# Kernel optimization log

Measured on AMD Instinct MI355X. Metric: run time of the kernel, lower is better.

The kernel has to match this reference:

```python
import jax, jax.numpy as jnp
import numpy as np

S, N, DIN, DH, C, K, E = 12, 50000, 64, 128, 2, 3, 600000
HID = (DH + C) // 2  # 65
LN_EPS = 1e-5


def setup_inputs() -> dict:
    key = jax.random.key(0)
    ks = jax.random.split(key, 16)
    sc = 0.05
    inp = {
        'H': jax.random.normal(ks[0], (S, N, DIN), dtype=jnp.float32),
        'edge_index': jax.random.randint(ks[1], (2, E), 0, N, dtype=jnp.int64),
        # stacked gate params, gate order: 0=i, 1=f, 2=c(cell), 3=o
        'Wx': jax.random.normal(ks[2], (4, K, DIN, DH), dtype=jnp.float32) * sc,
        'bx': jnp.zeros((4, DH), dtype=jnp.float32),
        'Wh': jax.random.normal(ks[3], (4, K, DH, DH), dtype=jnp.float32) * sc,
        'bh': jnp.zeros((4, DH), dtype=jnp.float32),
        'b_gate': jnp.zeros((4, DH), dtype=jnp.float32),
        'wc': jax.random.normal(ks[4], (3, DH), dtype=jnp.float32) * sc,  # peephole: i, f, o
        'ln_gamma': jnp.ones((DH,), dtype=jnp.float32),
        'ln_beta': jnp.zeros((DH,), dtype=jnp.float32),
        'W1': jax.random.normal(ks[5], (DH, HID), dtype=jnp.float32) * sc,
        'b1': jnp.zeros((HID,), dtype=jnp.float32),
        'W2': jax.random.normal(ks[6], (HID, C), dtype=jnp.float32) * sc,
        'b2': jnp.zeros((C,), dtype=jnp.float32),
    }
    return inp


def _cheb_norm(edge_index):
    # sym-normalized, lambda_max=2 => scaled Laplacian Lhat = -D^-1/2 A D^-1/2 (zero diagonal)
    src, dst = edge_index[0], edge_index[1]
    ones = jnp.ones((src.shape[0],), dtype=jnp.float32)
    deg = jax.ops.segment_sum(ones, src, num_segments=N)
    dinv = jnp.where(deg > 0, jax.lax.rsqrt(jnp.maximum(deg, 1.0)), 0.0)
    norm = -dinv[src] * dinv[dst]
    return src, dst, norm


def _cheb_conv(x, W, b, src, dst, norm):
    # x: [N, Din]; W: [K, Din, Dout]. T0=x, T1=Lhat x, Tk=2 Lhat T_{k-1} - T_{k-2}
    Tx0 = x
    out = Tx0 @ W[0]
    if K > 1:
        Tx1 = jax.ops.segment_sum(norm[:, None] * Tx0[src], dst, num_segments=N)
        out = out + Tx1 @ W[1]
        for k in range(2, K):
            Tx2 = 2.0 * jax.ops.segment_sum(norm[:, None] * Tx1[src], dst, num_segments=N) - Tx0
            out = out + Tx2 @ W[k]
            Tx0, Tx1 = Tx1, Tx2
    return out + b


def _decoder(H, edge_index, Wx, bx, Wh, bh, b_gate, wc, ln_gamma, ln_beta, W1, b1, W2, b2):
    src, dst, norm = _cheb_norm(edge_index)

    def step(carry, x_t):
        h, c = carry
        gx = lambda g: _cheb_conv(x_t, Wx[g], bx[g], src, dst, norm)
        gh = lambda g: _cheb_conv(h, Wh[g], bh[g], src, dst, norm)
        i = jax.nn.sigmoid(gx(0) + gh(0) + wc[0] * c + b_gate[0])
        f = jax.nn.sigmoid(gx(1) + gh(1) + wc[1] * c + b_gate[1])
        t = jnp.tanh(gx(2) + gh(2) + b_gate[2])
        c = f * c + i * t
        o = jax.nn.sigmoid(gx(3) + gh(3) + wc[2] * c + b_gate[3])
        h = o * jnp.tanh(c)
        return (h, c), h

    h0 = jnp.zeros((N, DH), dtype=H.dtype)
    (_, _), X = jax.lax.scan(step, (h0, h0), H)  # X: [S, N, DH]

    X = jnp.tanh(X)
    # LayerNorm over conv_dim (last axis here)
    mu = jnp.mean(X, axis=-1, keepdims=True)
    var = jnp.mean(jnp.square(X - mu), axis=-1, keepdims=True)
    X = (X - mu) * jax.lax.rsqrt(var + LN_EPS) * ln_gamma + ln_beta
    # dropout in eval mode: identity
    X = jax.nn.relu(X @ W1 + b1) @ W2 + b2  # [S, N, C]
    X = jax.nn.sigmoid(X)
    return jnp.transpose(X, (1, 2, 0))  # [N, C, S]


def reference(H, edge_index, Wx, bx, Wh, bh, b_gate, wc, ln_gamma, ln_beta, W1, b1, W2, b2):
    return _decoder(H, edge_index, Wx, bx, Wh, bh, b_gate, wc, ln_gamma, ln_beta, W1, b1, W2, b2)
```

## Files before the change

kernel.cpp:

```cpp
#include <hip/hip_runtime.h>
#include <cstdint>
#include <cstddef>

#define S_DIM 12
#define N_NODE 50000
#define N_PAD 50048
#define N_P2 50176
#define D_IN 64
#define D_H 128
#define N_E 600000
#define K_TOT 576
#define N_COL 512
#define HID_P 80
#define N_HID 65
#define AXC 192

typedef short bf16x8 __attribute__((ext_vector_type(8)));
typedef float f32x4 __attribute__((ext_vector_type(4)));

__device__ __forceinline__ float bf2f(unsigned short u){
  union { unsigned int i; float f; } v; v.i = ((unsigned int)u) << 16; return v.f;
}
__device__ __forceinline__ unsigned short f2bf(float f){
  union { float f; unsigned int i; } v; v.f = f;
  unsigned int x = v.i;
  return (unsigned short)((x + 0x7fffu + ((x >> 16) & 1u)) >> 16);
}
__device__ __forceinline__ float sigf(float x){ return 1.f/(1.f + __expf(-x)); }
__device__ __forceinline__ float ftanh(float x){
  x = fminf(fmaxf(x, -12.f), 12.f);
  float e = __expf(2.f*x);
  return (e - 1.f)/(e + 1.f);
}

__device__ __forceinline__ void gload16(const void* g, void* lds){
  __builtin_amdgcn_global_load_lds((const __attribute__((address_space(1))) unsigned int*)g,
                                   (__attribute__((address_space(3))) unsigned int*)lds, 16, 0, 0);
}

__device__ __forceinline__ void acc12(float* a, uint2 p0, uint2 p1, uint2 p2, float w){
  unsigned int u[6] = {p0.x, p0.y, p1.x, p1.y, p2.x, p2.y};
#pragma unroll
  for (int i=0;i<6;++i){
    a[2*i]   += w * bf2f((unsigned short)(u[i] & 0xffffu));
    a[2*i+1] += w * bf2f((unsigned short)(u[i] >> 16));
  }
}
__device__ __forceinline__ void acc8(float* a, uint4 h, float w){
  unsigned int u[4] = {h.x, h.y, h.z, h.w};
#pragma unroll
  for (int i=0;i<4;++i){
    a[2*i]   += w * bf2f((unsigned short)(u[i] & 0xffffu));
    a[2*i+1] += w * bf2f((unsigned short)(u[i] >> 16));
  }
}

__global__ void k_prep(const float* __restrict__ Wx, const float* __restrict__ Wh,
                       const float* __restrict__ bx, const float* __restrict__ bh,
                       const float* __restrict__ bg, const float* __restrict__ W1,
                       const float* __restrict__ b1, const float* __restrict__ W2,
                       unsigned short* __restrict__ Bct, float* __restrict__ btot,
                       unsigned short* __restrict__ W1t, float* __restrict__ b1p,
                       float* __restrict__ W2p)
{
  int idx = blockIdx.x*256 + threadIdx.x;
  if (idx < N_COL*K_TOT){
    int cc = idx / K_TOT, k = idx - cc*K_TOT;
    int g = (cc>>4)&3, d = (cc&15) + ((cc>>6)<<4);
    float v;
    if (k < 384){
      int kt = k >> 7, j = k & 127;
      const float* Wg = Wh + (size_t)g*3*128*128;
      if (kt == 0)      v = Wg[(size_t)j*128 + d] - Wg[(size_t)(256+j)*128 + d];
      else if (kt == 1) v = Wg[(size_t)(128+j)*128 + d];
      else              v = 2.f*Wg[(size_t)(256+j)*128 + d];
    } else {
      int kk = k - 384; int kt = kk >> 6, j = kk & 63;
      const float* Wg = Wx + (size_t)g*3*64*128;
      if (kt == 0)      v = Wg[(size_t)j*128 + d] - Wg[(size_t)(128+j)*128 + d];
      else if (kt == 1) v = Wg[(size_t)(64+j)*128 + d];
      else              v = 2.f*Wg[(size_t)(128+j)*128 + d];
    }
    Bct[(size_t)cc*K_TOT + k] = f2bf(v);
  }
  if (idx < N_COL) btot[idx] = bx[idx] + bh[idx] + bg[idx];
  if (idx < HID_P*D_H){ int c = idx >> 7, k = idx & 127;
    W1t[idx] = (c < N_HID) ? f2bf(W1[k*N_HID + c]) : (unsigned short)0; }
  if (idx < HID_P) b1p[idx] = (idx < N_HID) ? b1[idx] : 0.f;
  if (idx < HID_P*2){ int c = idx >> 1, j = idx & 1; W2p[idx] = (c < N_HID) ? W2[c*2 + j] : 0.f; }
}

__global__ void k_xprep(const float* __restrict__ H, unsigned short* __restrict__ Xtr,
                        unsigned short* __restrict__ Axt){
  int idx = blockIdx.x*256 + threadIdx.x;
  if (idx >= N_PAD*64) return;
  int n = idx >> 6, d = idx & 63;
  union { unsigned short u[12]; uint2 q[3]; } pk;
  if (n < N_NODE){
#pragma unroll
    for (int t=0;t<12;++t) pk.u[t] = f2bf(H[((size_t)t*N_NODE + n)*64 + d]);
  } else {
#pragma unroll
    for (int t=0;t<12;++t) pk.u[t] = 0;
  }
  uint2* xp = (uint2*)(Xtr + (size_t)idx*12);
  xp[0]=pk.q[0]; xp[1]=pk.q[1]; xp[2]=pk.q[2];
#pragma unroll
  for (int t=0;t<12;++t) Axt[((size_t)t*N_PAD + n)*AXC + d] = pk.u[t];
  if (n >= N_NODE){
#pragma unroll
    for (int t=0;t<12;++t){
      Axt[((size_t)t*N_PAD + n)*AXC + 64 + d]  = 0;
      Axt[((size_t)t*N_PAD + n)*AXC + 128 + d] = 0;
    }
  }
}

__global__ void k_deg(const int* __restrict__ ei, int* __restrict__ dsrc, int* __restrict__ ddst){
  int e = blockIdx.x*256 + threadIdx.x;
  if (e < N_E){
    atomicAdd(&dsrc[ei[e]], 1);
    atomicAdd(&ddst[ei[N_E + e]], 1);
  }
}
__global__ void k_dinv(const int* __restrict__ dsrc, float* __restrict__ dinv){
  int n = blockIdx.x*256 + threadIdx.x;
  if (n < N_P2) dinv[n] = (dsrc[n] > 0) ? rsqrtf((float)dsrc[n]) : 0.f;
}
__global__ void k_scan1(const int* __restrict__ in, int* __restrict__ outp, int* __restrict__ part){
  __shared__ int sm[256];
  int tid = threadIdx.x;
  int i = blockIdx.x*256 + tid;
  int v = in[i];
  int x = v;
  sm[tid] = x; __syncthreads();
  for (int off=1; off<256; off<<=1){
    int y = (tid >= off) ? sm[tid-off] : 0;
    __syncthreads();
    x += y; sm[tid] = x; __syncthreads();
  }
  outp[i] = x - v;
  if (tid == 255) part[blockIdx.x] = x;
}
__global__ void k_scan2(int* __restrict__ part, int nblk){
  __shared__ int sm[256];
  int tid = threadIdx.x;
  int v = (tid < nblk) ? part[tid] : 0;
  int x = v; sm[tid] = x; __syncthreads();
  for (int off=1; off<256; off<<=1){
    int y = (tid >= off) ? sm[tid-off] : 0;
    __syncthreads();
    x += y; sm[tid] = x; __syncthreads();
  }
  if (tid < nblk) part[tid] = x - v;
}
__global__ void k_scan3(const int* __restrict__ outp, const int* __restrict__ part, int* __restrict__ offs){
  int i = blockIdx.x*256 + threadIdx.x;
  offs[i] = outp[i] + part[blockIdx.x];
}
__global__ void k_csr(const int* __restrict__ ei, const float* __restrict__ dinv,
                      const int* __restrict__ offs, int* __restrict__ cursor,
                      int2* __restrict__ cedge){
  int e = blockIdx.x*256 + threadIdx.x;
  if (e < N_E){
    int s = ei[e], d = ei[N_E + e];
    int pos = atomicAdd(&cursor[d], 1);
    float w = -dinv[s]*dinv[d];
    cedge[offs[d] + pos] = make_int2(s, __float_as_int(w));
  }
}

__global__ void k_xspmm1(const unsigned short* __restrict__ Xtr, unsigned short* __restrict__ Axt,
                         unsigned short* __restrict__ U1tr,
                         const int* __restrict__ offs, const int2* __restrict__ cedge){
  int n = blockIdx.x*4 + (threadIdx.x >> 6);
  int l = threadIdx.x & 63;
  if (n >= N_NODE) return;
  int beg = offs[n], end = offs[n+1];
  float a[12];
#pragma unroll
  for (int t=0;t<12;++t) a[t] = 0.f;
  for (int q = beg; q < end; q += 3){
    int2 e0 = cedge[q];
    int2 e1 = (q+1 < end) ? cedge[q+1] : make_int2(0,0);
    int2 e2 = (q+2 < end) ? cedge[q+2] : make_int2(0,0);
    const uint2* r0 = (const uint2*)(Xtr + ((size_t)e0.x*64 + l)*12);
    const uint2* r1 = (const uint2*)(Xtr + ((size_t)e1.x*64 + l)*12);
    const uint2* r2 = (const uint2*)(Xtr + ((size_t)e2.x*64 + l)*12);
    uint2 p00=r0[0], p01=r0[1], p02=r0[2];
    uint2 p10=r1[0], p11=r1[1], p12=r1[2];
    uint2 p20=r2[0], p21=r2[1], p22=r2[2];
    acc12(a, p00, p01, p02, __int_as_float(e0.y));
    acc12(a, p10, p11, p12, __int_as_float(e1.y));
    acc12(a, p20, p21, p22, __int_as_float(e2.y));
  }
  union { unsigned short u[12]; uint2 qq[3]; } pk;
#pragma unroll
  for (int t=0;t<12;++t){
    unsigned short b = f2bf(a[t]);
    pk.u[t] = b;
    Axt[((size_t)t*N_PAD + n)*AXC + 64 + l] = b;
  }
  uint2* op = (uint2*)(U1tr + ((size_t)n*64 + l)*12);
  op[0]=pk.qq[0]; op[1]=pk.qq[1]; op[2]=pk.qq[2];
}
__global__ void k_xspmm2(const unsigned short* __restrict__ U1tr, unsigned short* __restrict__ Axt,
                         const int* __restrict__ offs, const int2* __restrict__ cedge){
  int n = blockIdx.x*4 + (threadIdx.x >> 6);
  int l = threadIdx.x & 63;
  if (n >= N_NODE) return;
  int beg = offs[n], end = offs[n+1];
  float a[12];
#pragma unroll
  for (int t=0;t<12;++t) a[t] = 0.f;
  for (int q = beg; q < end; q += 3){
    int2 e0 = cedge[q];
    int2 e1 = (q+1 < end) ? cedge[q+1] : make_int2(0,0);
    int2 e2 = (q+2 < end) ? cedge[q+2] : make_int2(0,0);
    const uint2* r0 = (const uint2*)(U1tr + ((size_t)e0.x*64 + l)*12);
    const uint2* r1 = (const uint2*)(U1tr + ((size_t)e1.x*64 + l)*12);
    const uint2* r2 = (const uint2*)(U1tr + ((size_t)e2.x*64 + l)*12);
    uint2 p00=r0[0], p01=r0[1], p02=r0[2];
    uint2 p10=r1[0], p11=r1[1], p12=r1[2];
    uint2 p20=r2[0], p21=r2[1], p22=r2[2];
    acc12(a, p00, p01, p02, __int_as_float(e0.y));
    acc12(a, p10, p11, p12, __int_as_float(e1.y));
    acc12(a, p20, p21, p22, __int_as_float(e2.y));
  }
#pragma unroll
  for (int t=0;t<12;++t)
    Axt[((size_t)t*N_PAD + n)*AXC + 128 + l] = f2bf(a[t]);
}

__global__ void k_spmm1(const unsigned short* __restrict__ Hc, unsigned short* __restrict__ U,
                        const int* __restrict__ offs, const int2* __restrict__ cedge){
  int n = blockIdx.x*4 + (threadIdx.x >> 6);
  int l = threadIdx.x & 63;
  if (n >= N_NODE) return;
  int sub = l >> 4, fl = l & 15;
  int beg = offs[n], end = offs[n+1];
  float a[8];
#pragma unroll
  for (int j=0;j<8;++j) a[j] = 0.f;
  for (int q = beg; q < end; q += 8){
    int i0 = q + sub, i1 = q + 4 + sub;
    int2 e0 = (i0 < end) ? cedge[i0] : make_int2(0,0);
    int2 e1 = (i1 < end) ? cedge[i1] : make_int2(0,0);
    uint4 h0 = *(const uint4*)(Hc + (size_t)e0.x*128 + fl*8);
    uint4 h1 = *(const uint4*)(Hc + (size_t)e1.x*128 + fl*8);
    acc8(a, h0, __int_as_float(e0.y));
    acc8(a, h1, __int_as_float(e1.y));
  }
#pragma unroll
  for (int j=0;j<8;++j){
    a[j] += __shfl_xor(a[j], 16);
    a[j] += __shfl_xor(a[j], 32);
  }
  if (sub == 0){
    unsigned short o[8];
#pragma unroll
    for (int j=0;j<8;++j) o[j] = f2bf(a[j]);
    *(uint4*)(U + (size_t)n*256 + fl*8) = *(const uint4*)o;
  }
}
__global__ void k_spmm2(unsigned short* __restrict__ U,
                        const int* __restrict__ offs, const int2* __restrict__ cedge){
  int n = blockIdx.x*4 + (threadIdx.x >> 6);
  int l = threadIdx.x & 63;
  if (n >= N_NODE) return;
  int sub = l >> 4, fl = l & 15;
  int beg = offs[n], end = offs[n+1];
  float a[8];
#pragma unroll
  for (int j=0;j<8;++j) a[j] = 0.f;
  for (int q = beg; q < end; q += 8){
    int i0 = q + sub, i1 = q + 4 + sub;
    int2 e0 = (i0 < end) ? cedge[i0] : make_int2(0,0);
    int2 e1 = (i1 < end) ? cedge[i1] : make_int2(0,0);
    uint4 h0 = *(const uint4*)(U + (size_t)e0.x*256 + fl*8);
    uint4 h1 = *(const uint4*)(U + (size_t)e1.x*256 + fl*8);
    acc8(a, h0, __int_as_float(e0.y));
    acc8(a, h1, __int_as_float(e1.y));
  }
#pragma unroll
  for (int j=0;j<8;++j){
    a[j] += __shfl_xor(a[j], 16);
    a[j] += __shfl_xor(a[j], 32);
  }
  if (sub == 0){
    unsigned short o[8];
#pragma unroll
    for (int j=0;j<8;++j) o[j] = f2bf(a[j]);
    *(uint4*)(U + (size_t)n*256 + 128 + fl*8) = *(const uint4*)o;
  }
}

__global__ __launch_bounds__(256,2) void k_gemm(
    const unsigned short* __restrict__ Hc, const unsigned short* __restrict__ U,
    const unsigned short* __restrict__ Axt,
    const unsigned short* __restrict__ Bct, const float* __restrict__ btot,
    const float* __restrict__ wc, float* __restrict__ c, unsigned short* __restrict__ Hn)
{
  __shared__ __align__(16) unsigned short As[128*64];
  __shared__ __align__(16) unsigned short Bs[128*64];
  int tid = threadIdx.x;
  int w = tid >> 6, l = tid & 63;
  const int NWG = 1564, q8 = NWG >> 3, r8 = NWG & 7;
  int L = blockIdx.y*4 + blockIdx.x;
  int xcd = L & 7, li = L >> 3;
  int W = (xcd < r8 ? xcd*(q8+1) : r8*(q8+1) + (xcd-r8)*q8) + li;
  int bx = W & 3, by = W >> 2;
  int n0 = bx * 128;
  int m0 = by * 128;
  const f32x4 vzero = {0.f,0.f,0.f,0.f};
  f32x4 acc[4][4];
#pragma unroll
  for (int i=0;i<4;++i)
#pragma unroll
    for (int j=0;j<4;++j) acc[i][j] = vzero;
  int wr = w >> 1, wn = w & 1;
  for (int it=0; it<9; ++it){
    const unsigned short* Ab; int astr, acol;
    if (it < 2)      { Ab = Hc;  astr = 128; acol = it*64; }
    else if (it < 6) { Ab = U;   astr = 256; acol = (it-2)*64; }
    else             { Ab = Axt; astr = AXC; acol = (it-6)*64; }
    if (it) __syncthreads();
#pragma unroll
    for (int i=0;i<4;++i){
      int rr = w*32 + i*8;
      int row = rr + (l>>3);
      gload16(Ab  + (size_t)(m0+row)*astr + acol + (l&7)*8, (void*)(As + rr*64));
      gload16(Bct + (size_t)(n0+row)*K_TOT + it*64 + (l&7)*8, (void*)(Bs + rr*64));
    }
    __syncthreads();
#pragma unroll
    for (int kk=0; kk<2; ++kk){
      bf16x8 af[4], bfv[4];
#pragma unroll
      for (int i=0;i<4;++i) af[i]  = *(const bf16x8*)(As + (wr*64 + i*16 + (l&15))*64 + kk*32 + (l>>4)*8);
#pragma unroll
      for (int j=0;j<4;++j) bfv[j] = *(const bf16x8*)(Bs + (wn*64 + j*16 + (l&15))*64 + kk*32 + (l>>4)*8);
#pragma unroll
      for (int i=0;i<4;++i)
#pragma unroll
        for (int j=0;j<4;++j)
          acc[i][j] = __builtin_amdgcn_mfma_f32_16x16x32_bf16(af[i], bfv[j], acc[i][j], 0,0,0);
    }
  }
  int dd = (((bx<<1) + wn) << 4) | (l & 15);
  float b_i = btot[dd], b_f = btot[128+dd], b_t = btot[256+dd], b_o = btot[384+dd];
  float wci = wc[dd], wcf = wc[128+dd], wco = wc[256+dd];
#pragma unroll
  for (int i=0;i<4;++i){
    int row0 = m0 + wr*64 + i*16 + (l>>4)*4;
#pragma unroll
    for (int r=0;r<4;++r){
      int row = row0 + r;
      float co = c[(size_t)row*128 + dd];
      float gi = sigf(acc[i][0][r] + b_i + wci*co);
      float gf = sigf(acc[i][1][r] + b_f + wcf*co);
      float tt = ftanh(acc[i][2][r] + b_t);
      float cn = gf*co + gi*tt;
      float go = sigf(acc[i][3][r] + b_o + wco*cn);
      float h = go * ftanh(cn);
      c[(size_t)row*128 + dd] = cn;
      Hn[(size_t)row*128 + dd] = f2bf(h);
    }
  }
}

__global__ __launch_bounds__(256,2) void k_lnmlp(const unsigned short* __restrict__ Hn,
                        const unsigned short* __restrict__ W1t, const float* __restrict__ b1p,
                        const float* __restrict__ W2p, const float* __restrict__ b2,
                        const float* __restrict__ gam, const float* __restrict__ bet,
                        float* __restrict__ out, int t)
{
  __shared__ __align__(16) unsigned short xn[64*128];
  __shared__ __align__(16) unsigned short w1s[HID_P*128];
  __shared__ float w2s[HID_P*2];
  __shared__ float b1s[HID_P];
  __shared__ float b2s[2];
  int tid = threadIdx.x;
  for (int i = tid; i < HID_P*128/8; i += 256) ((int4*)w1s)[i] = ((const int4*)W1t)[i];
  if (tid < HID_P*2) w2s[tid] = W2p[tid];
  if (tid < HID_P)   b1s[tid] = b1p[tid];
  if (tid < 2)       b2s[tid] = b2[tid];
  int n0 = blockIdx.x*64;
  int row = tid >> 2, part = tid & 3;
  int n = n0 + row;
  float vals[32];
  float s = 0.f, ss = 0.f;
  if (n < N_NODE){
    const unsigned short* hp = Hn + (size_t)n*128 + part*32;
#pragma unroll
    for (int k=0;k<32;++k){
      float x = ftanh(bf2f(hp[k]));
      vals[k] = x; s += x; ss += x*x;
    }
  } else {
#pragma unroll
    for (int k=0;k<32;++k) vals[k] = 0.f;
  }
  s  += __shfl_xor(s,1);  s  += __shfl_xor(s,2);
  ss += __shfl_xor(ss,1); ss += __shfl_xor(ss,2);
  float mu = s * (1.f/128.f);
  float var = ss * (1.f/128.f) - mu*mu;
  float inv = rsqrtf(fmaxf(var, 0.f) + 1e-5f);
#pragma unroll
  for (int k=0;k<32;++k){
    int d = part*32 + k;
    xn[row*128 + d] = f2bf((vals[k]-mu)*inv*gam[d] + bet[d]);
  }
  __syncthreads();
  int w = tid >> 6, l = tid & 63;
  const f32x4 vzero = {0.f,0.f,0.f,0.f};
  f32x4 acc[5];
#pragma unroll
  for (int tj=0;tj<5;++tj) acc[tj] = vzero;
#pragma unroll
  for (int kk=0;kk<4;++kk){
    bf16x8 a = *(const bf16x8*)(xn + (w*16 + (l&15))*128 + kk*32 + (l>>4)*8);
#pragma unroll
    for (int tj=0;tj<5;++tj){
      bf16x8 b = *(const bf16x8*)(w1s + (tj*16 + (l&15))*128 + kk*32 + (l>>4)*8);
      acc[tj] = __builtin_amdgcn_mfma_f32_16x16x32_bf16(a, b, acc[tj], 0,0,0);
    }
  }
#pragma unroll
  for (int r=0;r<4;++r){
    int rn = n0 + w*16 + (l>>4)*4 + r;
    float p0 = 0.f, p1 = 0.f;
#pragma unroll
    for (int tj=0;tj<5;++tj){
      int col = tj*16 + (l&15);
      float hv = fmaxf(acc[tj][r] + b1s[col], 0.f);
      p0 += hv * w2s[col*2];
      p1 += hv * w2s[col*2+1];
    }
    p0 += __shfl_xor(p0,1); p0 += __shfl_xor(p0,2); p0 += __shfl_xor(p0,4); p0 += __shfl_xor(p0,8);
    p1 += __shfl_xor(p1,1); p1 += __shfl_xor(p1,2); p1 += __shfl_xor(p1,4); p1 += __shfl_xor(p1,8);
    if ((l & 15) == 0 && rn < N_NODE){
      float* op = out + (size_t)rn*24 + t;
      op[0]  = sigf(p0 + b2s[0]);
      op[12] = sigf(p1 + b2s[1]);
    }
  }
}

extern "C" void kernel_launch(void* const* d_in, const int* in_sizes, int n_in,
                              void* d_out, int out_size, void* d_ws, size_t ws_size,
                              hipStream_t stream)
{
  const float* H   = (const float*)d_in[0];
  const int*   ei  = (const int*)d_in[1];
  const float* Wx  = (const float*)d_in[2];
  const float* bx  = (const float*)d_in[3];
  const float* Wh  = (const float*)d_in[4];
  const float* bh  = (const float*)d_in[5];
  const float* bg  = (const float*)d_in[6];
  const float* wc  = (const float*)d_in[7];
  const float* gam = (const float*)d_in[8];
  const float* bet = (const float*)d_in[9];
  const float* W1  = (const float*)d_in[10];
  const float* b1  = (const float*)d_in[11];
  const float* W2  = (const float*)d_in[12];
  const float* b2  = (const float*)d_in[13];
  float* out = (float*)d_out;
  (void)in_sizes; (void)n_in; (void)out_size; (void)ws_size;

  char* p = (char*)d_ws;
  auto alloc = [&](size_t bytes)->char*{ char* r = p; p += (bytes + 255) & ~(size_t)255; return r; };
  char* zbase = p;
  float*          c_st  = (float*)alloc((size_t)N_PAD*128*4);
  unsigned short* Hbuf0 = (unsigned short*)alloc((size_t)N_PAD*128*2);
  int* dsrc   = (int*)alloc((size_t)N_P2*4);
  int* ddst   = (int*)alloc((size_t)N_P2*4);
  int* cursor = (int*)alloc((size_t)N_P2*4);
  size_t zbytes = (size_t)(p - zbase);
  unsigned short* Hbuf1 = (unsigned short*)alloc((size_t)N_PAD*128*2);
  unsigned short* Ubuf  = (unsigned short*)alloc((size_t)N_PAD*256*2);
  unsigned short* Xtr   = (unsigned short*)alloc((size_t)N_PAD*64*12*2);
  unsigned short* U1tr  = (unsigned short*)alloc((size_t)N_PAD*64*12*2);
  unsigned short* Axt   = (unsigned short*)alloc((size_t)S_DIM*N_PAD*AXC*2);
  unsigned short* Bct   = (unsigned short*)alloc((size_t)N_COL*K_TOT*2);
  float*          btot  = (float*)alloc(N_COL*4);
  unsigned short* W1t   = (unsigned short*)alloc(HID_P*128*2);
  float*          b1p   = (float*)alloc(HID_P*4);
  float*          W2p   = (float*)alloc(HID_P*2*4);
  float*          dinv  = (float*)alloc((size_t)N_P2*4);
  int*            offs  = (int*)alloc((size_t)(N_P2+256)*4);
  int*            outp  = (int*)alloc((size_t)N_P2*4);
  int*            partb = (int*)alloc(256*4);
  int2*           cedge = (int2*)alloc((size_t)N_E*8);

  hipMemsetAsync(zbase, 0, zbytes, stream);
  k_prep<<<(N_COL*K_TOT + 255)/256, 256, 0, stream>>>(Wx, Wh, bx, bh, bg, W1, b1, W2,
                                                      Bct, btot, W1t, b1p, W2p);
  k_xprep<<<(N_PAD*64 + 255)/256, 256, 0, stream>>>(H, Xtr, Axt);
  k_deg<<<(N_E + 255)/256, 256, 0, stream>>>(ei, dsrc, ddst);
  k_dinv<<<N_P2/256, 256, 0, stream>>>(dsrc, dinv);
  k_scan1<<<N_P2/256, 256, 0, stream>>>(ddst, outp, partb);
  k_scan2<<<1, 256, 0, stream>>>(partb, N_P2/256);
  k_scan3<<<N_P2/256, 256, 0, stream>>>(outp, partb, offs);
  k_csr<<<(N_E + 255)/256, 256, 0, stream>>>(ei, dinv, offs, cursor, cedge);
  k_xspmm1<<<N_NODE/4, 256, 0, stream>>>(Xtr, Axt, U1tr, offs, cedge);
  k_xspmm2<<<N_NODE/4, 256, 0, stream>>>(U1tr, Axt, offs, cedge);

  for (int t = 0; t < S_DIM; ++t){
    unsigned short* Hc = (t & 1) ? Hbuf1 : Hbuf0;
    unsigned short* Hn = (t & 1) ? Hbuf0 : Hbuf1;
    k_spmm1<<<N_NODE/4, 256, 0, stream>>>(Hc, Ubuf, offs, cedge);
    k_spmm2<<<N_NODE/4, 256, 0, stream>>>(Ubuf, offs, cedge);
    k_gemm<<<dim3(4, N_PAD/128), 256, 0, stream>>>(Hc, Ubuf,
        Axt + (size_t)t*N_PAD*AXC, Bct, btot, wc, c_st, Hn);
    k_lnmlp<<<N_PAD/64, 256, 0, stream>>>(Hn, W1t, b1p, W2p, b2, gam, bet, out, t);
  }
}
```

Measured before the change: 1.973 ms.

## Unroll SpMM gathers, double-buffer GEMM LDS tiles, skip first-step hidden SpMM

The CSR gather loops in the four SpMM kernels now process twice as many edges per iteration, using clamped indices and zeroed weights in place of conditional loads, so more gathers are in flight. The GEMM gets double-buffered shared-memory tiles so the next K-slice loads while MFMAs run on the current one, with one barrier per iteration. At t=0 the hidden-state SpMMs are skipped because h0 is zero, and Ubuf is moved into the memset region so its zeros stand in for them. The trade-off is more registers and twice the LDS per block, which may lower occupancy under launch_bounds(256,2).

```diff
diff --git a/kernel.cpp b/kernel.cpp
--- a/kernel.cpp
+++ b/kernel.cpp
@@ -177,22 +177,41 @@
   int l = threadIdx.x & 63;
   if (n >= N_NODE) return;
   int beg = offs[n], end = offs[n+1];
+  int ce = end - 1;
   float a[12];
 #pragma unroll
   for (int t=0;t<12;++t) a[t] = 0.f;
-  for (int q = beg; q < end; q += 3){
-    int2 e0 = cedge[q];
-    int2 e1 = (q+1 < end) ? cedge[q+1] : make_int2(0,0);
-    int2 e2 = (q+2 < end) ? cedge[q+2] : make_int2(0,0);
+  for (int q = beg; q < end; q += 6){
+    int2 e0 = cedge[min(q,   ce)];
+    int2 e1 = cedge[min(q+1, ce)];
+    int2 e2 = cedge[min(q+2, ce)];
+    int2 e3 = cedge[min(q+3, ce)];
+    int2 e4 = cedge[min(q+4, ce)];
+    int2 e5 = cedge[min(q+5, ce)];
+    float w0 = __int_as_float(e0.y);
+    float w1 = (q+1 < end) ? __int_as_float(e1.y) : 0.f;
+    float w2 = (q+2 < end) ? __int_as_float(e2.y) : 0.f;
+    float w3 = (q+3 < end) ? __int_as_float(e3.y) : 0.f;
+    float w4 = (q+4 < end) ? __int_as_float(e4.y) : 0.f;
+    float w5 = (q+5 < end) ? __int_as_float(e5.y) : 0.f;
     const uint2* r0 = (const uint2*)(Xtr + ((size_t)e0.x*64 + l)*12);
     const uint2* r1 = (const uint2*)(Xtr + ((size_t)e1.x*64 + l)*12);
     const uint2* r2 = (const uint2*)(Xtr + ((size_t)e2.x*64 + l)*12);
+    const uint2* r3 = (const uint2*)(Xtr + ((size_t)e3.x*64 + l)*12);
+    const uint2* r4 = (const uint2*)(Xtr + ((size_t)e4.x*64 + l)*12);
+    const uint2* r5 = (const uint2*)(Xtr + ((size_t)e5.x*64 + l)*12);
     uint2 p00=r0[0], p01=r0[1], p02=r0[2];
     uint2 p10=r1[0], p11=r1[1], p12=r1[2];
     uint2 p20=r2[0], p21=r2[1], p22=r2[2];
-    acc12(a, p00, p01, p02, __int_as_float(e0.y));
-    acc12(a, p10, p11, p12, __int_as_float(e1.y));
-    acc12(a, p20, p21, p22, __int_as_float(e2.y));
+    uint2 p30=r3[0], p31=r3[1], p32=r3[2];
+    uint2 p40=r4[0], p41=r4[1], p42=r4[2];
+    uint2 p50=r5[0], p51=r5[1], p52=r5[2];
+    acc12(a, p00, p01, p02, w0);
+    acc12(a, p10, p11, p12, w1);
+    acc12(a, p20, p21, p22, w2);
+    acc12(a, p30, p31, p32, w3);
+    acc12(a, p40, p41, p42, w4);
+    acc12(a, p50, p51, p52, w5);
   }
   union { unsigned short u[12]; uint2 qq[3]; } pk;
 #pragma unroll
@@ -210,22 +229,41 @@
   int l = threadIdx.x & 63;
   if (n >= N_NODE) return;
   int beg = offs[n], end = offs[n+1];
+  int ce = end - 1;
   float a[12];
 #pragma unroll
   for (int t=0;t<12;++t) a[t] = 0.f;
-  for (int q = beg; q < end; q += 3){
-    int2 e0 = cedge[q];
-    int2 e1 = (q+1 < end) ? cedge[q+1] : make_int2(0,0);
-    int2 e2 = (q+2 < end) ? cedge[q+2] : make_int2(0,0);
+  for (int q = beg; q < end; q += 6){
+    int2 e0 = cedge[min(q,   ce)];
+    int2 e1 = cedge[min(q+1, ce)];
+    int2 e2 = cedge[min(q+2, ce)];
+    int2 e3 = cedge[min(q+3, ce)];
+    int2 e4 = cedge[min(q+4, ce)];
+    int2 e5 = cedge[min(q+5, ce)];
+    float w0 = __int_as_float(e0.y);
+    float w1 = (q+1 < end) ? __int_as_float(e1.y) : 0.f;
+    float w2 = (q+2 < end) ? __int_as_float(e2.y) : 0.f;
+    float w3 = (q+3 < end) ? __int_as_float(e3.y) : 0.f;
+    float w4 = (q+4 < end) ? __int_as_float(e4.y) : 0.f;
+    float w5 = (q+5 < end) ? __int_as_float(e5.y) : 0.f;
     const uint2* r0 = (const uint2*)(U1tr + ((size_t)e0.x*64 + l)*12);
     const uint2* r1 = (const uint2*)(U1tr + ((size_t)e1.x*64 + l)*12);
     const uint2* r2 = (const uint2*)(U1tr + ((size_t)e2.x*64 + l)*12);
+    const uint2* r3 = (const uint2*)(U1tr + ((size_t)e3.x*64 + l)*12);
+    const uint2* r4 = (const uint2*)(U1tr + ((size_t)e4.x*64 + l)*12);
+    const uint2* r5 = (const uint2*)(U1tr + ((size_t)e5.x*64 + l)*12);
     uint2 p00=r0[0], p01=r0[1], p02=r0[2];
     uint2 p10=r1[0], p11=r1[1], p12=r1[2];
     uint2 p20=r2[0], p21=r2[1], p22=r2[2];
-    acc12(a, p00, p01, p02, __int_as_float(e0.y));
-    acc12(a, p10, p11, p12, __int_as_float(e1.y));
-    acc12(a, p20, p21, p22, __int_as_float(e2.y));
+    uint2 p30=r3[0], p31=r3[1], p32=r3[2];
+    uint2 p40=r4[0], p41=r4[1], p42=r4[2];
+    uint2 p50=r5[0], p51=r5[1], p52=r5[2];
+    acc12(a, p00, p01, p02, w0);
+    acc12(a, p10, p11, p12, w1);
+    acc12(a, p20, p21, p22, w2);
+    acc12(a, p30, p31, p32, w3);
+    acc12(a, p40, p41, p42, w4);
+    acc12(a, p50, p51, p52, w5);
   }
 #pragma unroll
   for (int t=0;t<12;++t)
@@ -239,17 +277,28 @@
   if (n >= N_NODE) return;
   int sub = l >> 4, fl = l & 15;
   int beg = offs[n], end = offs[n+1];
+  int ce = end - 1;
   float a[8];
 #pragma unroll
   for (int j=0;j<8;++j) a[j] = 0.f;
-  for (int q = beg; q < end; q += 8){
-    int i0 = q + sub, i1 = q + 4 + sub;
-    int2 e0 = (i0 < end) ? cedge[i0] : make_int2(0,0);
-    int2 e1 = (i1 < end) ? cedge[i1] : make_int2(0,0);
+  for (int q = beg; q < end; q += 16){
+    int i0 = q + sub, i1 = q + 4 + sub, i2 = q + 8 + sub, i3 = q + 12 + sub;
+    int2 e0 = cedge[min(i0, ce)];
+    int2 e1 = cedge[min(i1, ce)];
+    int2 e2 = cedge[min(i2, ce)];
+    int2 e3 = cedge[min(i3, ce)];
+    float w0 = (i0 < end) ? __int_as_float(e0.y) : 0.f;
+    float w1 = (i1 < end) ? __int_as_float(e1.y) : 0.f;
+    float w2 = (i2 < end) ? __int_as_float(e2.y) : 0.f;
+    float w3 = (i3 < end) ? __int_as_float(e3.y) : 0.f;
     uint4 h0 = *(const uint4*)(Hc + (size_t)e0.x*128 + fl*8);
     uint4 h1 = *(const uint4*)(Hc + (size_t)e1.x*128 + fl*8);
-    acc8(a, h0, __int_as_float(e0.y));
-    acc8(a, h1, __int_as_float(e1.y));
+    uint4 h2 = *(const uint4*)(Hc + (size_t)e2.x*128 + fl*8);
+    uint4 h3 = *(const uint4*)(Hc + (size_t)e3.x*128 + fl*8);
+    acc8(a, h0, w0);
+    acc8(a, h1, w1);
+    acc8(a, h2, w2);
+    acc8(a, h3, w3);
   }
 #pragma unroll
   for (int j=0;j<8;++j){
@@ -270,17 +319,28 @@
   if (n >= N_NODE) return;
   int sub = l >> 4, fl = l & 15;
   int beg = offs[n], end = offs[n+1];
+  int ce = end - 1;
   float a[8];
 #pragma unroll
   for (int j=0;j<8;++j) a[j] = 0.f;
-  for (int q = beg; q < end; q += 8){
-    int i0 = q + sub, i1 = q + 4 + sub;
-    int2 e0 = (i0 < end) ? cedge[i0] : make_int2(0,0);
-    int2 e1 = (i1 < end) ? cedge[i1] : make_int2(0,0);
+  for (int q = beg; q < end; q += 16){
+    int i0 = q + sub, i1 = q + 4 + sub, i2 = q + 8 + sub, i3 = q + 12 + sub;
+    int2 e0 = cedge[min(i0, ce)];
+    int2 e1 = cedge[min(i1, ce)];
+    int2 e2 = cedge[min(i2, ce)];
+    int2 e3 = cedge[min(i3, ce)];
+    float w0 = (i0 < end) ? __int_as_float(e0.y) : 0.f;
+    float w1 = (i1 < end) ? __int_as_float(e1.y) : 0.f;
+    float w2 = (i2 < end) ? __int_as_float(e2.y) : 0.f;
+    float w3 = (i3 < end) ? __int_as_float(e3.y) : 0.f;
     uint4 h0 = *(const uint4*)(U + (size_t)e0.x*256 + fl*8);
     uint4 h1 = *(const uint4*)(U + (size_t)e1.x*256 + fl*8);
-    acc8(a, h0, __int_as_float(e0.y));
-    acc8(a, h1, __int_as_float(e1.y));
+    uint4 h2 = *(const uint4*)(U + (size_t)e2.x*256 + fl*8);
+    uint4 h3 = *(const uint4*)(U + (size_t)e3.x*256 + fl*8);
+    acc8(a, h0, w0);
+    acc8(a, h1, w1);
+    acc8(a, h2, w2);
+    acc8(a, h3, w3);
   }
 #pragma unroll
   for (int j=0;j<8;++j){
@@ -301,8 +361,8 @@
     const unsigned short* __restrict__ Bct, const float* __restrict__ btot,
     const float* __restrict__ wc, float* __restrict__ c, unsigned short* __restrict__ Hn)
 {
-  __shared__ __align__(16) unsigned short As[128*64];
-  __shared__ __align__(16) unsigned short Bs[128*64];
+  __shared__ __align__(16) unsigned short As[2][128*64];
+  __shared__ __align__(16) unsigned short Bs[2][128*64];
   int tid = threadIdx.x;
   int w = tid >> 6, l = tid & 63;
   const int NWG = 1564, q8 = NWG >> 3, r8 = NWG & 7;
@@ -319,33 +379,40 @@
 #pragma unroll
     for (int j=0;j<4;++j) acc[i][j] = vzero;
   int wr = w >> 1, wn = w & 1;
-  for (int it=0; it<9; ++it){
+
+  auto stage = [&](int buf, int it){
     const unsigned short* Ab; int astr, acol;
     if (it < 2)      { Ab = Hc;  astr = 128; acol = it*64; }
     else if (it < 6) { Ab = U;   astr = 256; acol = (it-2)*64; }
     else             { Ab = Axt; astr = AXC; acol = (it-6)*64; }
-    if (it) __syncthreads();
 #pragma unroll
     for (int i=0;i<4;++i){
       int rr = w*32 + i*8;
       int row = rr + (l>>3);
-      gload16(Ab  + (size_t)(m0+row)*astr + acol + (l&7)*8, (void*)(As + rr*64));
-      gload16(Bct + (size_t)(n0+row)*K_TOT + it*64 + (l&7)*8, (void*)(Bs + rr*64));
-    }
-    __syncthreads();
+      gload16(Ab  + (size_t)(m0+row)*astr + acol + (l&7)*8, (void*)(As[buf] + rr*64));
+      gload16(Bct + (size_t)(n0+row)*K_TOT + it*64 + (l&7)*8, (void*)(Bs[buf] + rr*64));
+    }
+  };
+
+  stage(0, 0);
+  __syncthreads();
+  for (int it=0; it<9; ++it){
+    int cur = it & 1;
+    if (it < 8) stage(cur^1, it+1);
 #pragma unroll
     for (int kk=0; kk<2; ++kk){
       bf16x8 af[4], bfv[4];
 #pragma unroll
-      for (int i=0;i<4;++i) af[i]  = *(const bf16x8*)(As + (wr*64 + i*16 + (l&15))*64 + kk*32 + (l>>4)*8);
-#pragma unroll
-      for (int j=0;j<4;++j) bfv[j] = *(const bf16x8*)(Bs + (wn*64 + j*16 + (l&15))*64 + kk*32 + (l>>4)*8);
+      for (int i=0;i<4;++i) af[i]  = *(const bf16x8*)(As[cur] + (wr*64 + i*16 + (l&15))*64 + kk*32 + (l>>4)*8);
+#pragma unroll
+      for (int j=0;j<4;++j) bfv[j] = *(const bf16x8*)(Bs[cur] + (wn*64 + j*16 + (l&15))*64 + kk*32 + (l>>4)*8);
 #pragma unroll
       for (int i=0;i<4;++i)
 #pragma unroll
         for (int j=0;j<4;++j)
           acc[i][j] = __builtin_amdgcn_mfma_f32_16x16x32_bf16(af[i], bfv[j], acc[i][j], 0,0,0);
     }
+    __syncthreads();
   }
   int dd = (((bx<<1) + wn) << 4) | (l & 15);
   float b_i = btot[dd], b_f = btot[128+dd], b_t = btot[256+dd], b_o = btot[384+dd];
@@ -473,12 +540,12 @@
   char* zbase = p;
   float*          c_st  = (float*)alloc((size_t)N_PAD*128*4);
   unsigned short* Hbuf0 = (unsigned short*)alloc((size_t)N_PAD*128*2);
+  unsigned short* Ubuf  = (unsigned short*)alloc((size_t)N_PAD*256*2);
   int* dsrc   = (int*)alloc((size_t)N_P2*4);
   int* ddst   = (int*)alloc((size_t)N_P2*4);
   int* cursor = (int*)alloc((size_t)N_P2*4);
   size_t zbytes = (size_t)(p - zbase);
   unsigned short* Hbuf1 = (unsigned short*)alloc((size_t)N_PAD*128*2);
-  unsigned short* Ubuf  = (unsigned short*)alloc((size_t)N_PAD*256*2);
   unsigned short* Xtr   = (unsigned short*)alloc((size_t)N_PAD*64*12*2);
   unsigned short* U1tr  = (unsigned short*)alloc((size_t)N_PAD*64*12*2);
   unsigned short* Axt   = (unsigned short*)alloc((size_t)S_DIM*N_PAD*AXC*2);
@@ -509,8 +576,10 @@
   for (int t = 0; t < S_DIM; ++t){
     unsigned short* Hc = (t & 1) ? Hbuf1 : Hbuf0;
     unsigned short* Hn = (t & 1) ? Hbuf0 : Hbuf1;
-    k_spmm1<<<N_NODE/4, 256, 0, stream>>>(Hc, Ubuf, offs, cedge);
-    k_spmm2<<<N_NODE/4, 256, 0, stream>>>(Ubuf, offs, cedge);
+    if (t > 0){
+      k_spmm1<<<N_NODE/4, 256, 0, stream>>>(Hc, Ubuf, offs, cedge);
+      k_spmm2<<<N_NODE/4, 256, 0, stream>>>(Ubuf, offs, cedge);
+    }
     k_gemm<<<dim3(4, N_PAD/128), 256, 0, stream>>>(Hc, Ubuf,
         Axt + (size_t)t*N_PAD*AXC, Bct, btot, wc, c_st, Hn);
     k_lnmlp<<<N_PAD/64, 256, 0, stream>>>(Hn, W1t, b1p, W2p, b2, gam, bet, out, t);
```

Result: no change. 1.976 ms (+0.2%).
